# Kernel tuning notes

Hardware: AMD Instinct MI355X
Metric: run time of the kernel (lower is better)

The kernel has to match this reference:

```python
import jax, jax.numpy as jnp
import numpy as np

N = 50000        # nodes
E = 800000       # edges (before self-loops)
F_IN = 128       # num_features
HID = 32         # hidden_size per head
HEADS = 4
CLS = 40         # num_classes
NEG_SLOPE = 0.2  # PyG GATConv default leaky_relu slope


def setup_inputs() -> dict:
    key = jax.random.key(0)
    ks = jax.random.split(key, 10)
    s = lambda k, sh: (jax.random.normal(k, sh, jnp.float32) * 0.05)
    x = jax.random.normal(ks[0], (N, F_IN), jnp.float32)
    edge_index = jax.random.randint(ks[1], (2, E), 0, N, dtype=jnp.int64)
    W1 = s(ks[2], (F_IN, HEADS * HID))
    att_src1 = s(ks[3], (HEADS, HID))
    att_dst1 = s(ks[4], (HEADS, HID))
    b1 = jnp.zeros((HEADS * HID,), jnp.float32)
    W2 = s(ks[5], (HEADS * HID, CLS))
    att_src2 = s(ks[6], (1, CLS))
    att_dst2 = s(ks[7], (1, CLS))
    b2 = jnp.zeros((CLS,), jnp.float32)
    return {"x": x, "edge_index": edge_index, "W1": W1, "att_src1": att_src1,
            "att_dst1": att_dst1, "b1": b1, "W2": W2, "att_src2": att_src2,
            "att_dst2": att_dst2, "b2": b2}


def _add_self_loops(edge_index, num_nodes):
    ar = jnp.arange(num_nodes, dtype=edge_index.dtype)
    loops = jnp.stack([ar, ar])
    return jnp.concatenate([edge_index, loops], axis=1)


def _gat_conv(x, edge_index, W, a_src, a_dst, bias, heads, concat):
    """PyG GATConv (eval mode, additive attention, self-loops already added)."""
    n = x.shape[0]
    src, dst = edge_index[0], edge_index[1]
    h = (x @ W).reshape(n, heads, -1)                 # [N, H, C]
    a_s = jnp.einsum('nhc,hc->nh', h, a_src)          # [N, H]
    a_d = jnp.einsum('nhc,hc->nh', h, a_dst)          # [N, H]
    e = jax.nn.leaky_relu(a_s[src] + a_d[dst], NEG_SLOPE)   # [E', H]
    m = jax.ops.segment_max(e, dst, num_segments=n)   # segment softmax over dst
    ex = jnp.exp(e - m[dst])
    den = jax.ops.segment_sum(ex, dst, num_segments=n)
    alpha = ex / den[dst]                             # [E', H]
    out = jax.ops.segment_sum(h[src] * alpha[:, :, None], dst, num_segments=n)
    out = out.reshape(n, -1) if concat else out.mean(axis=1)
    return out + bias


def reference(x, edge_index, W1, att_src1, att_dst1, b1, W2, att_src2, att_dst2, b2):
    ei = _add_self_loops(edge_index, x.shape[0])
    # dropout p=0 in eval -> identity
    h = jax.nn.relu(_gat_conv(x, ei, W1, att_src1, att_dst1, b1, HEADS, True))
    out = _gat_conv(h, ei, W2, att_src2, att_dst2, b2, 1, True)  # heads=1
    return out
```

## Files before the change

### kernel.cpp

```cpp
#include <hip/hip_runtime.h>
#include <cstdint>

#define NODES 50000
#define FIN   128
#define C1    128
#define HEADS 4
#define HID   32
#define CLS   40
#define SLOPE 0.2f

#define NBUCK ((NODES + 255) >> 8)
#define EPB 2048
#define BCAP 8192

__device__ __forceinline__ float lrelu(float v) { return v > 0.f ? v : SLOPE * v; }

__device__ __forceinline__ unsigned short f2bf(float f) {
    union { float f; unsigned u; } v; v.f = f;
    unsigned u = v.u;
    return (unsigned short)((u + 0x7FFFu + ((u >> 16) & 1u)) >> 16);
}
__device__ __forceinline__ float bf2f(unsigned short b) {
    union { unsigned u; float f; } v; v.u = ((unsigned)b) << 16;
    return v.f;
}
__device__ __forceinline__ float bflo(unsigned u) {
    union { unsigned x; float f; } v; v.x = u << 16; return v.f;
}
__device__ __forceinline__ float bfhi(unsigned u) {
    union { unsigned x; float f; } v; v.x = u & 0xffff0000u; return v.f;
}

typedef __attribute__((ext_vector_type(8))) short bf16x8;
typedef __attribute__((ext_vector_type(4))) float f32x4;
typedef __attribute__((ext_vector_type(4), aligned(4))) int int4a;
typedef __attribute__((ext_vector_type(2), aligned(4))) int int2a;

__global__ __launch_bounds__(256) void k_prep(const float* __restrict__ W1,
                                              const float* __restrict__ W2,
                                              unsigned short* __restrict__ w1t,
                                              unsigned short* __restrict__ w2t,
                                              int* __restrict__ bwp) {
    __shared__ unsigned short Tb[128][136];
    const int t = threadIdx.x;
#pragma unroll
    for (int i = 0; i < 64; i++) {
        int p = i * 256 + t;
        int k = p >> 7, n = p & 127;
        Tb[n][k] = f2bf(W1[(size_t)k * C1 + n]);
    }
    __syncthreads();
#pragma unroll
    for (int i = 0; i < 8; i++) {
        int p = i * 256 + t;
        int n = p >> 4, k8 = (p & 15) * 8;
        *(uint4*)(w1t + n * 128 + k8) = *(uint4*)(&Tb[n][k8]);
    }
    for (int p = t; p < CLS * 128; p += 256) {
        int n = p >> 7, k = p & 127;
        w2t[n * 128 + k] = f2bf(W2[(size_t)k * CLS + n]);
    }
    if (t < NBUCK) bwp[t] = t * BCAP;
}

__global__ __launch_bounds__(256) void k_gemm1(const float* __restrict__ X,
                                               const unsigned short* __restrict__ w1t,
                                               const float* __restrict__ AS,
                                               const float* __restrict__ AD,
                                               unsigned short* __restrict__ h1b,
                                               float* __restrict__ as1,
                                               float* __restrict__ ad1) {
    __shared__ unsigned short Asm[64][136];
    __shared__ unsigned short Wt[128][136];
    const int t = threadIdx.x;
    const int row0 = blockIdx.x * 64;

#pragma unroll
    for (int i = 0; i < 8; i++) {
        int p = i * 256 + t;
        int n = p >> 4, k8 = (p & 15) * 8;
        *(uint4*)(&Wt[n][k8]) = *(const uint4*)(w1t + n * 128 + k8);
    }
    {
        int r = t >> 2, c0 = (t & 3) * 32;
        int gr = row0 + r;
        unsigned short tb[32];
        if (gr < NODES) {
#pragma unroll
            for (int i = 0; i < 8; i++) {
                float4 v = *(const float4*)(X + (size_t)gr * FIN + c0 + i * 4);
                tb[i * 4 + 0] = f2bf(v.x); tb[i * 4 + 1] = f2bf(v.y);
                tb[i * 4 + 2] = f2bf(v.z); tb[i * 4 + 3] = f2bf(v.w);
            }
        } else {
#pragma unroll
            for (int i = 0; i < 32; i++) tb[i] = 0;
        }
#pragma unroll
        for (int i = 0; i < 4; i++) {
            uint4 pk;
            pk.x = (unsigned)tb[i*8+0] | ((unsigned)tb[i*8+1] << 16);
            pk.y = (unsigned)tb[i*8+2] | ((unsigned)tb[i*8+3] << 16);
            pk.z = (unsigned)tb[i*8+4] | ((unsigned)tb[i*8+5] << 16);
            pk.w = (unsigned)tb[i*8+6] | ((unsigned)tb[i*8+7] << 16);
            *(uint4*)(&Asm[r][c0 + i * 8]) = pk;
        }
    }
    __syncthreads();

    const int w = t >> 6, l = t & 63;
    const int lm = l & 15, quad = l >> 4;
    f32x4 acc[8];
#pragma unroll
    for (int ct = 0; ct < 8; ct++) acc[ct] = (f32x4){0.f, 0.f, 0.f, 0.f};
#pragma unroll
    for (int kt = 0; kt < 4; kt++) {
        bf16x8 a = *(const bf16x8*)(&Asm[w * 16 + lm][kt * 32 + quad * 8]);
#pragma unroll
        for (int ct = 0; ct < 8; ct++) {
            bf16x8 b = *(const bf16x8*)(&Wt[ct * 16 + lm][kt * 32 + quad * 8]);
            acc[ct] = __builtin_amdgcn_mfma_f32_16x16x32_bf16(a, b, acc[ct], 0, 0, 0);
        }
    }
    __syncthreads();
#pragma unroll
    for (int ct = 0; ct < 8; ct++)
#pragma unroll
        for (int r = 0; r < 4; r++)
            Asm[w * 16 + quad * 4 + r][ct * 16 + lm] = f2bf(acc[ct][r]);
    __syncthreads();
    {
        int r = t >> 2, c0 = (t & 3) * 32;
        int gr = row0 + r;
        if (gr < NODES) {
#pragma unroll
            for (int i = 0; i < 4; i++)
                *(uint4*)(h1b + (size_t)gr * C1 + c0 + i * 8) =
                    *(uint4*)(&Asm[r][c0 + i * 8]);
        }
    }
    {
        int r = t >> 2, h = t & 3;
        int gr = row0 + r;
        if (gr < NODES) {
            float s = 0.f, d = 0.f;
#pragma unroll
            for (int j = 0; j < 32; j++) {
                float v = bf2f(Asm[r][h * 32 + j]);
                s = fmaf(v, AS[h * HID + j], s);
                d = fmaf(v, AD[h * HID + j], d);
            }
            as1[gr * HEADS + h] = s;
            ad1[gr * HEADS + h] = d;
        }
    }
}

__global__ __launch_bounds__(256) void k_bucketA(const int* __restrict__ src,
                                                 const int* __restrict__ dst, int E,
                                                 int* __restrict__ bwp,
                                                 int* __restrict__ tmp) {
    __shared__ int cnt[NBUCK];
    __shared__ int bbs[NBUCK];
    const int t = threadIdx.x;
    for (int i = t; i < NBUCK; i += 256) cnt[i] = 0;
    __syncthreads();
    const int e0 = blockIdx.x * EPB;
    int v[8], rb[8];
#pragma unroll
    for (int k = 0; k < 8; k++) {
        int e = e0 + k * 256 + t;
        rb[k] = -1;
        if (e < E) {
            int d = dst[e], s = src[e];
            int b = d >> 8;
            int r = atomicAdd(&cnt[b], 1);
            v[k] = (s << 8) | (d & 255);
            rb[k] = (r << 8) | b;
        }
    }
    __syncthreads();
    for (int i = t; i < NBUCK; i += 256) {
        int c = cnt[i];
        bbs[i] = c ? atomicAdd(&bwp[i], c) : 0;
    }
    __syncthreads();
#pragma unroll
    for (int k = 0; k < 8; k++) {
        if (rb[k] >= 0) {
            int b = rb[k] & 255;
            int r = rb[k] >> 8;
            tmp[bbs[b] + r] = v[k];
        }
    }
}

__global__ __launch_bounds__(256) void k_bucketB(const int* __restrict__ bwp,
                                                 const int* __restrict__ tmp,
                                                 int* __restrict__ col,
                                                 int* __restrict__ rowptr,
                                                 int* __restrict__ degarr) {
    __shared__ int degs[256];
    __shared__ int wp[256];
    __shared__ int wsum[4];
    const int b = blockIdx.x, t = threadIdx.x;
    const int n0 = b << 8;
    const int beg = b * BCAP;
    const int end = bwp[b];
    degs[t] = 0;
    __syncthreads();
    for (int e = beg + t; e < end; e += 256)
        atomicAdd(&degs[tmp[e] & 255], 1);
    __syncthreads();
    const int d = degs[t];
    int incl = d;
    const int lane = t & 63, w = t >> 6;
#pragma unroll
    for (int s = 1; s < 64; s <<= 1) {
        int u = __shfl_up(incl, s);
        if (lane >= s) incl += u;
    }
    if (lane == 63) wsum[w] = incl;
    __syncthreads();
    if (t == 0) {
        int r = 0;
#pragma unroll
        for (int i = 0; i < 4; i++) { int x = wsum[i]; wsum[i] = r; r += x; }
    }
    __syncthreads();
    const int excl = incl - d + wsum[w] + beg;
    const int nidx = n0 + t;
    if (nidx < NODES) { rowptr[nidx] = excl; degarr[nidx] = d; }
    wp[t] = excl;
    __syncthreads();
    for (int e = beg + t; e < end; e += 256) {
        int v = tmp[e];
        int p = atomicAdd(&wp[v & 255], 1);
        col[p] = v >> 8;
    }
}

__global__ __launch_bounds__(256) void k_agg1(const unsigned short* __restrict__ h1b,
                                              const float* __restrict__ as1,
                                              const float* __restrict__ ad1,
                                              const int* __restrict__ rowptr,
                                              const int* __restrict__ degarr,
                                              const int* __restrict__ col,
                                              const float* __restrict__ b1,
                                              unsigned short* __restrict__ out1) {
    int wid = (blockIdx.x * 256 + threadIdx.x) >> 6;
    if (wid >= NODES) return;
    const int lane = threadIdx.x & 63;
    const int q  = lane >> 4;
    const int ll = lane & 15;
    const int fh = ll >> 2;
    const int n = wid;
    const float adn = ad1[n * HEADS + fh];
    const int rs = rowptr[n];
    const int re = rs + degarr[n];

    float den = 0.f;
    float ac[8];
#pragma unroll
    for (int k = 0; k < 8; k++) ac[k] = 0.f;

    int base = rs;
    for (; base + 16 <= re; base += 16) {
        int4a cc = *(const int4a*)(col + base + q * 4);
        float w0 = __expf(lrelu(as1[cc.x * HEADS + fh] + adn));
        float w1 = __expf(lrelu(as1[cc.y * HEADS + fh] + adn));
        float w2 = __expf(lrelu(as1[cc.z * HEADS + fh] + adn));
        float w3 = __expf(lrelu(as1[cc.w * HEADS + fh] + adn));
        den += (w0 + w1) + (w2 + w3);
        uint4 p0 = *(const uint4*)((const char*)h1b + (((unsigned)cc.x << 8) + (unsigned)(ll << 4)));
        uint4 p1 = *(const uint4*)((const char*)h1b + (((unsigned)cc.y << 8) + (unsigned)(ll << 4)));
        uint4 p2 = *(const uint4*)((const char*)h1b + (((unsigned)cc.z << 8) + (unsigned)(ll << 4)));
        uint4 p3 = *(const uint4*)((const char*)h1b + (((unsigned)cc.w << 8) + (unsigned)(ll << 4)));
        ac[0] = fmaf(w0, bflo(p0.x), ac[0]); ac[1] = fmaf(w0, bfhi(p0.x), ac[1]);
        ac[2] = fmaf(w0, bflo(p0.y), ac[2]); ac[3] = fmaf(w0, bfhi(p0.y), ac[3]);
        ac[4] = fmaf(w0, bflo(p0.z), ac[4]); ac[5] = fmaf(w0, bfhi(p0.z), ac[5]);
        ac[6] = fmaf(w0, bflo(p0.w), ac[6]); ac[7] = fmaf(w0, bfhi(p0.w), ac[7]);
        ac[0] = fmaf(w1, bflo(p1.x), ac[0]); ac[1] = fmaf(w1, bfhi(p1.x), ac[1]);
        ac[2] = fmaf(w1, bflo(p1.y), ac[2]); ac[3] = fmaf(w1, bfhi(p1.y), ac[3]);
        ac[4] = fmaf(w1, bflo(p1.z), ac[4]); ac[5] = fmaf(w1, bfhi(p1.z), ac[5]);
        ac[6] = fmaf(w1, bflo(p1.w), ac[6]); ac[7] = fmaf(w1, bfhi(p1.w), ac[7]);
        ac[0] = fmaf(w2, bflo(p2.x), ac[0]); ac[1] = fmaf(w2, bfhi(p2.x), ac[1]);
        ac[2] = fmaf(w2, bflo(p2.y), ac[2]); ac[3] = fmaf(w2, bfhi(p2.y), ac[3]);
        ac[4] = fmaf(w2, bflo(p2.z), ac[4]); ac[5] = fmaf(w2, bfhi(p2.z), ac[5]);
        ac[6] = fmaf(w2, bflo(p2.w), ac[6]); ac[7] = fmaf(w2, bfhi(p2.w), ac[7]);
        ac[0] = fmaf(w3, bflo(p3.x), ac[0]); ac[1] = fmaf(w3, bfhi(p3.x), ac[1]);
        ac[2] = fmaf(w3, bflo(p3.y), ac[2]); ac[3] = fmaf(w3, bfhi(p3.y), ac[3]);
        ac[4] = fmaf(w3, bflo(p3.z), ac[4]); ac[5] = fmaf(w3, bfhi(p3.z), ac[5]);
        ac[6] = fmaf(w3, bflo(p3.w), ac[6]); ac[7] = fmaf(w3, bfhi(p3.w), ac[7]);
    }
    for (; base < re; base += 4) {
        int i = base + q;
        int c = (i < re) ? col[i] : n;
        float w = __expf(lrelu(as1[c * HEADS + fh] + adn));
        if (i >= re) w = 0.f;
        den += w;
        unsigned off = ((unsigned)c << 8) + (unsigned)(ll << 4);
        uint4 pk = *(const uint4*)((const char*)h1b + off);
        ac[0] = fmaf(w, bflo(pk.x), ac[0]); ac[1] = fmaf(w, bfhi(pk.x), ac[1]);
        ac[2] = fmaf(w, bflo(pk.y), ac[2]); ac[3] = fmaf(w, bfhi(pk.y), ac[3]);
        ac[4] = fmaf(w, bflo(pk.z), ac[4]); ac[5] = fmaf(w, bfhi(pk.z), ac[5]);
        ac[6] = fmaf(w, bflo(pk.w), ac[6]); ac[7] = fmaf(w, bfhi(pk.w), ac[7]);
    }
    den += __shfl_xor(den, 16);
    den += __shfl_xor(den, 32);
#pragma unroll
    for (int k = 0; k < 8; k++) {
        ac[k] += __shfl_xor(ac[k], 16);
        ac[k] += __shfl_xor(ac[k], 32);
    }
    const float wself = __expf(lrelu(as1[n * HEADS + fh] + adn));
    den += wself;
    if (q == 0) {
        unsigned offs = ((unsigned)n << 8) + (unsigned)(ll << 4);
        uint4 sp = *(const uint4*)((const char*)h1b + offs);
        float sv[8] = {bflo(sp.x), bfhi(sp.x), bflo(sp.y), bfhi(sp.y),
                       bflo(sp.z), bfhi(sp.z), bflo(sp.w), bfhi(sp.w)};
        float4 bv0 = *(const float4*)(b1 + ll * 8);
        float4 bv1 = *(const float4*)(b1 + ll * 8 + 4);
        float bb[8] = {bv0.x, bv0.y, bv0.z, bv0.w, bv1.x, bv1.y, bv1.z, bv1.w};
        unsigned short ob[8];
#pragma unroll
        for (int k = 0; k < 8; k++)
            ob[k] = f2bf(fmaxf((ac[k] + wself * sv[k]) / den + bb[k], 0.f));
        uint4 pk;
        pk.x = (unsigned)ob[0] | ((unsigned)ob[1] << 16);
        pk.y = (unsigned)ob[2] | ((unsigned)ob[3] << 16);
        pk.z = (unsigned)ob[4] | ((unsigned)ob[5] << 16);
        pk.w = (unsigned)ob[6] | ((unsigned)ob[7] << 16);
        *(uint4*)(out1 + (size_t)n * C1 + ll * 8) = pk;
    }
}

__global__ __launch_bounds__(256) void k_gemm2(const unsigned short* __restrict__ out1b,
                                               const unsigned short* __restrict__ w2t,
                                               const float* __restrict__ AS,
                                               const float* __restrict__ AD,
                                               unsigned short* __restrict__ h2b,
                                               float* __restrict__ as2,
                                               float* __restrict__ ad2) {
    __shared__ unsigned short Asm[64][136];
    __shared__ unsigned short Wt2[48][136];
    __shared__ float Cc[64][52];
    const int t = threadIdx.x;
    const int row0 = blockIdx.x * 64;

    for (int p = t; p < 8 * 136; p += 256) Wt2[40 + p / 136][p % 136] = 0;
    for (int p = t; p < 640; p += 256) {
        int n = p >> 4, k8 = (p & 15) * 8;
        *(uint4*)(&Wt2[n][k8]) = *(const uint4*)(w2t + n * 128 + k8);
    }
    {
        int r = t >> 2, c0 = (t & 3) * 32;
        int gr = row0 + r;
        if (gr < NODES) {
#pragma unroll
            for (int i = 0; i < 4; i++)
                *(uint4*)(&Asm[r][c0 + i * 8]) =
                    *(const uint4*)(out1b + (size_t)gr * C1 + c0 + i * 8);
        } else {
            uint4 z = make_uint4(0, 0, 0, 0);
#pragma unroll
            for (int i = 0; i < 4; i++) *(uint4*)(&Asm[r][c0 + i * 8]) = z;
        }
    }
    __syncthreads();

    const int w = t >> 6, l = t & 63;
    const int lm = l & 15, quad = l >> 4;
    f32x4 acc[3];
#pragma unroll
    for (int ct = 0; ct < 3; ct++) acc[ct] = (f32x4){0.f, 0.f, 0.f, 0.f};
#pragma unroll
    for (int kt = 0; kt < 4; kt++) {
        bf16x8 a = *(const bf16x8*)(&Asm[w * 16 + lm][kt * 32 + quad * 8]);
#pragma unroll
        for (int ct = 0; ct < 3; ct++) {
            bf16x8 b = *(const bf16x8*)(&Wt2[ct * 16 + lm][kt * 32 + quad * 8]);
            acc[ct] = __builtin_amdgcn_mfma_f32_16x16x32_bf16(a, b, acc[ct], 0, 0, 0);
        }
    }
    __syncthreads();
#pragma unroll
    for (int ct = 0; ct < 3; ct++)
#pragma unroll
        for (int r = 0; r < 4; r++)
            Cc[w * 16 + quad * 4 + r][ct * 16 + lm] = acc[ct][r];
    __syncthreads();
    {
        int r = t >> 2, c0 = (t & 3) * 10;
        int gr = row0 + r;
        if (gr < NODES) {
#pragma unroll
            for (int i = 0; i < 5; i++) {
                int c = c0 + i * 2;
                unsigned pk = (unsigned)f2bf(Cc[r][c]) |
                              ((unsigned)f2bf(Cc[r][c + 1]) << 16);
                *(unsigned*)(h2b + (size_t)gr * 64 + c) = pk;
            }
            float s = 0.f, d = 0.f;
#pragma unroll
            for (int j = 0; j < 10; j++) {
                float v = Cc[r][c0 + j];
                s = fmaf(v, AS[c0 + j], s);
                d = fmaf(v, AD[c0 + j], d);
            }
            s += __shfl_xor(s, 1); s += __shfl_xor(s, 2);
            d += __shfl_xor(d, 1); d += __shfl_xor(d, 2);
            if ((t & 3) == 0) { as2[gr] = s; ad2[gr] = d; }
        }
    }
}

__global__ __launch_bounds__(256) void k_agg2(const unsigned short* __restrict__ h2b,
                                              const float* __restrict__ as2,
                                              const float* __restrict__ ad2,
                                              const int* __restrict__ rowptr,
                                              const int* __restrict__ degarr,
                                              const int* __restrict__ col,
                                              const float* __restrict__ b2,
                                              float* __restrict__ out) {
    int wid = (blockIdx.x * 256 + threadIdx.x) >> 6;
    if (wid >= NODES) return;
    const int lane = threadIdx.x & 63;
    const int q8 = lane >> 3, l8 = lane & 7;
    const int n = wid;
    const float adn = ad2[n];
    const int rs = rowptr[n];
    const int re = rs + degarr[n];

    float den = 0.f;
    float ac[8];
#pragma unroll
    for (int k = 0; k < 8; k++) ac[k] = 0.f;

    int base = rs;
    for (; base + 16 <= re; base += 16) {
        int2a cc = *(const int2a*)(col + base + q8 * 2);
        float w0 = __expf(lrelu(as2[cc.x] + adn));
        float w1 = __expf(lrelu(as2[cc.y] + adn));
        den += w0 + w1;
        if (l8 < 5) {
            unsigned o0 = ((unsigned)cc.x << 7) + (unsigned)(l8 << 4);
            unsigned o1 = ((unsigned)cc.y << 7) + (unsigned)(l8 << 4);
            uint4 p0 = *(const uint4*)((const char*)h2b + o0);
            uint4 p1 = *(const uint4*)((const char*)h2b + o1);
            ac[0] = fmaf(w0, bflo(p0.x), ac[0]); ac[1] = fmaf(w0, bfhi(p0.x), ac[1]);
            ac[2] = fmaf(w0, bflo(p0.y), ac[2]); ac[3] = fmaf(w0, bfhi(p0.y), ac[3]);
            ac[4] = fmaf(w0, bflo(p0.z), ac[4]); ac[5] = fmaf(w0, bfhi(p0.z), ac[5]);
            ac[6] = fmaf(w0, bflo(p0.w), ac[6]); ac[7] = fmaf(w0, bfhi(p0.w), ac[7]);
            ac[0] = fmaf(w1, bflo(p1.x), ac[0]); ac[1] = fmaf(w1, bfhi(p1.x), ac[1]);
            ac[2] = fmaf(w1, bflo(p1.y), ac[2]); ac[3] = fmaf(w1, bfhi(p1.y), ac[3]);
            ac[4] = fmaf(w1, bflo(p1.z), ac[4]); ac[5] = fmaf(w1, bfhi(p1.z), ac[5]);
            ac[6] = fmaf(w1, bflo(p1.w), ac[6]); ac[7] = fmaf(w1, bfhi(p1.w), ac[7]);
        }
    }
    for (; base < re; base += 8) {
        int i = base + q8;
        int c = (i < re) ? col[i] : n;
        float w = __expf(lrelu(as2[c] + adn));
        if (i >= re) w = 0.f;
        den += w;
        if (l8 < 5) {
            unsigned off = ((unsigned)c << 7) + (unsigned)(l8 << 4);
            uint4 pk = *(const uint4*)((const char*)h2b + off);
            ac[0] = fmaf(w, bflo(pk.x), ac[0]); ac[1] = fmaf(w, bfhi(pk.x), ac[1]);
            ac[2] = fmaf(w, bflo(pk.y), ac[2]); ac[3] = fmaf(w, bfhi(pk.y), ac[3]);
            ac[4] = fmaf(w, bflo(pk.z), ac[4]); ac[5] = fmaf(w, bfhi(pk.z), ac[5]);
            ac[6] = fmaf(w, bflo(pk.w), ac[6]); ac[7] = fmaf(w, bfhi(pk.w), ac[7]);
        }
    }
    den += __shfl_xor(den, 8);
    den += __shfl_xor(den, 16);
    den += __shfl_xor(den, 32);
#pragma unroll
    for (int k = 0; k < 8; k++) {
        ac[k] += __shfl_xor(ac[k], 8);
        ac[k] += __shfl_xor(ac[k], 16);
        ac[k] += __shfl_xor(ac[k], 32);
    }
    const float wself = __expf(lrelu(as2[n] + adn));
    den += wself;
    if (q8 == 0 && l8 < 5) {
        unsigned offs = ((unsigned)n << 7) + (unsigned)(l8 << 4);
        uint4 sp = *(const uint4*)((const char*)h2b + offs);
        float sv[8] = {bflo(sp.x), bfhi(sp.x), bflo(sp.y), bfhi(sp.y),
                       bflo(sp.z), bfhi(sp.z), bflo(sp.w), bfhi(sp.w)};
        float4 bv0 = *(const float4*)(b2 + l8 * 8);
        float4 bv1 = *(const float4*)(b2 + l8 * 8 + 4);
        float bb[8] = {bv0.x, bv0.y, bv0.z, bv0.w, bv1.x, bv1.y, bv1.z, bv1.w};
        float o[8];
#pragma unroll
        for (int k = 0; k < 8; k++)
            o[k] = (ac[k] + wself * sv[k]) / den + bb[k];
        *(float4*)(out + (size_t)n * CLS + l8 * 8) =
            make_float4(o[0], o[1], o[2], o[3]);
        *(float4*)(out + (size_t)n * CLS + l8 * 8 + 4) =
            make_float4(o[4], o[5], o[6], o[7]);
    }
}

extern "C" void kernel_launch(void* const* d_in, const int* in_sizes, int n_in,
                              void* d_out, int out_size, void* d_ws, size_t ws_size,
                              hipStream_t stream) {
    const float* x     = (const float*)d_in[0];
    const int*   ei    = (const int*)d_in[1];
    const float* W1    = (const float*)d_in[2];
    const float* aS1   = (const float*)d_in[3];
    const float* aD1   = (const float*)d_in[4];
    const float* b1    = (const float*)d_in[5];
    const float* W2    = (const float*)d_in[6];
    const float* aS2   = (const float*)d_in[7];
    const float* aD2   = (const float*)d_in[8];
    const float* b2    = (const float*)d_in[9];
    float* out = (float*)d_out;
    const int E = in_sizes[1] / 2;
    const int* src = ei;
    const int* dst = ei + E;

    char* ws = (char*)d_ws;
    size_t off = 0;
    auto alloc = [&](size_t bytes) -> char* {
        char* p = ws + off;
        off += (bytes + 255) & ~(size_t)255;
        return p;
    };
    unsigned short* h1b  = (unsigned short*)alloc((size_t)NODES * C1 * 2);
    unsigned short* out1 = (unsigned short*)alloc((size_t)NODES * C1 * 2);
    unsigned short* h2b  = (unsigned short*)alloc((size_t)NODES * 64 * 2);
    float* as1    = (float*)alloc((size_t)NODES * HEADS * 4);
    float* ad1    = (float*)alloc((size_t)NODES * HEADS * 4);
    float* as2    = (float*)alloc((size_t)NODES * 4);
    float* ad2    = (float*)alloc((size_t)NODES * 4);
    int* rowptr   = (int*)alloc((size_t)NODES * 4);
    int* degarr   = (int*)alloc((size_t)NODES * 4);
    int* col      = (int*)alloc((size_t)NBUCK * BCAP * 4);
    int* tmp      = (int*)alloc((size_t)NBUCK * BCAP * 4);
    unsigned short* w1t = (unsigned short*)alloc((size_t)FIN * C1 * 2);
    unsigned short* w2t = (unsigned short*)alloc((size_t)CLS * 128 * 2);
    int* bwp      = (int*)alloc((size_t)NBUCK * 4);

    k_prep<<<1, 256, 0, stream>>>(W1, W2, w1t, w2t, bwp);
    k_gemm1<<<(NODES + 63) / 64, 256, 0, stream>>>(x, w1t, aS1, aD1, h1b, as1, ad1);
    k_bucketA<<<(E + EPB - 1) / EPB, 256, 0, stream>>>(src, dst, E, bwp, tmp);
    k_bucketB<<<NBUCK, 256, 0, stream>>>(bwp, tmp, col, rowptr, degarr);
    k_agg1<<<(NODES * 64) / 256, 256, 0, stream>>>(h1b, as1, ad1, rowptr, degarr, col, b1, out1);
    k_gemm2<<<(NODES + 63) / 64, 256, 0, stream>>>(out1, w2t, aS2, aD2, h2b, as2, ad2);
    k_agg2<<<(NODES * 64) / 256, 256, 0, stream>>>(h2b, as2, ad2, rowptr, degarr, col, b2, out);
}
```

Before: 211.9 us.

## Fuse edge bucketing into GEMM1 launch and fold GEMM2 into layer-1 aggregation

Edge bucketing (formerly its own kernel) now runs as extra blocks of the first GEMM kernel, so the two independent stages share one launch and can overlap. The second-layer projection and its attention scores are computed inside the layer-1 aggregation kernel: each wave shuffles its node's 128-wide bf16 output into an MFMA A-fragment with only one valid row and multiplies by W2 staged in shared memory. This removes the out1 intermediate round-trip through global memory and one kernel launch. The cost is that every aggregation block now loads W2 into shared memory, and the MFMA does mostly zero-padded work since only one of its 16 rows is a real node.

```diff
diff --git a/kernel.cpp b/kernel.cpp
--- a/kernel.cpp
+++ b/kernel.cpp
@@ -36,6 +36,8 @@
 typedef __attribute__((ext_vector_type(4), aligned(4))) int int4a;
 typedef __attribute__((ext_vector_type(2), aligned(4))) int int2a;
 
+union BF8 { uint4 u; bf16x8 v; };
+
 __global__ __launch_bounds__(256) void k_prep(const float* __restrict__ W1,
                                               const float* __restrict__ W2,
                                               unsigned short* __restrict__ w1t,
@@ -63,18 +65,58 @@
     if (t < NBUCK) bwp[t] = t * BCAP;
 }
 
-__global__ __launch_bounds__(256) void k_gemm1(const float* __restrict__ X,
+__global__ __launch_bounds__(256) void k_front(const float* __restrict__ X,
                                                const unsigned short* __restrict__ w1t,
                                                const float* __restrict__ AS,
                                                const float* __restrict__ AD,
                                                unsigned short* __restrict__ h1b,
                                                float* __restrict__ as1,
-                                               float* __restrict__ ad1) {
+                                               float* __restrict__ ad1,
+                                               const int* __restrict__ src,
+                                               const int* __restrict__ dst, int E,
+                                               int* __restrict__ bwp,
+                                               int* __restrict__ tmp, int GB1) {
     __shared__ unsigned short Asm[64][136];
     __shared__ unsigned short Wt[128][136];
+    __shared__ int cnt[NBUCK];
+    __shared__ int bbs[NBUCK];
     const int t = threadIdx.x;
+
+    if (blockIdx.x >= GB1) {
+        for (int i = t; i < NBUCK; i += 256) cnt[i] = 0;
+        __syncthreads();
+        const int e0 = (blockIdx.x - GB1) * EPB;
+        int v[8], rb[8];
+#pragma unroll
+        for (int k = 0; k < 8; k++) {
+            int e = e0 + k * 256 + t;
+            rb[k] = -1;
+            if (e < E) {
+                int d = dst[e], s = src[e];
+                int b = d >> 8;
+                int r = atomicAdd(&cnt[b], 1);
+                v[k] = (s << 8) | (d & 255);
+                rb[k] = (r << 8) | b;
+            }
+        }
+        __syncthreads();
+        for (int i = t; i < NBUCK; i += 256) {
+            int c = cnt[i];
+            bbs[i] = c ? atomicAdd(&bwp[i], c) : 0;
+        }
+        __syncthreads();
+#pragma unroll
+        for (int k = 0; k < 8; k++) {
+            if (rb[k] >= 0) {
+                int b = rb[k] & 255;
+                int r = rb[k] >> 8;
+                tmp[bbs[b] + r] = v[k];
+            }
+        }
+        return;
+    }
+
     const int row0 = blockIdx.x * 64;
-
 #pragma unroll
     for (int i = 0; i < 8; i++) {
         int p = i * 256 + t;
@@ -152,45 +194,6 @@
             }
             as1[gr * HEADS + h] = s;
             ad1[gr * HEADS + h] = d;
-        }
-    }
-}
-
-__global__ __launch_bounds__(256) void k_bucketA(const int* __restrict__ src,
-                                                 const int* __restrict__ dst, int E,
-                                                 int* __restrict__ bwp,
-                                                 int* __restrict__ tmp) {
-    __shared__ int cnt[NBUCK];
-    __shared__ int bbs[NBUCK];
-    const int t = threadIdx.x;
-    for (int i = t; i < NBUCK; i += 256) cnt[i] = 0;
-    __syncthreads();
-    const int e0 = blockIdx.x * EPB;
-    int v[8], rb[8];
-#pragma unroll
-    for (int k = 0; k < 8; k++) {
-        int e = e0 + k * 256 + t;
-        rb[k] = -1;
-        if (e < E) {
-            int d = dst[e], s = src[e];
-            int b = d >> 8;
-            int r = atomicAdd(&cnt[b], 1);
-            v[k] = (s << 8) | (d & 255);
-            rb[k] = (r << 8) | b;
-        }
-    }
-    __syncthreads();
-    for (int i = t; i < NBUCK; i += 256) {
-        int c = cnt[i];
-        bbs[i] = c ? atomicAdd(&bwp[i], c) : 0;
-    }
-    __syncthreads();
-#pragma unroll
-    for (int k = 0; k < 8; k++) {
-        if (rb[k] >= 0) {
-            int b = rb[k] & 255;
-            int r = rb[k] >> 8;
-            tmp[bbs[b] + r] = v[k];
         }
     }
 }
@@ -247,10 +250,23 @@
                                               const int* __restrict__ degarr,
                                               const int* __restrict__ col,
                                               const float* __restrict__ b1,
-                                              unsigned short* __restrict__ out1) {
-    int wid = (blockIdx.x * 256 + threadIdx.x) >> 6;
-    if (wid >= NODES) return;
-    const int lane = threadIdx.x & 63;
+                                              const unsigned short* __restrict__ w2t,
+                                              const float* __restrict__ AS2,
+                                              const float* __restrict__ AD2,
+                                              unsigned short* __restrict__ h2b,
+                                              float* __restrict__ as2,
+                                              float* __restrict__ ad2) {
+    __shared__ unsigned short Wt2[48][136];
+    const int t = threadIdx.x;
+    for (int p = t; p < 640; p += 256) {
+        int nn = p >> 4, k8 = (p & 15) * 8;
+        *(uint4*)(&Wt2[nn][k8]) = *(const uint4*)(w2t + nn * 128 + k8);
+    }
+    for (int p = t; p < 8 * 136; p += 256) Wt2[40 + p / 136][p % 136] = 0;
+    __syncthreads();
+
+    int wid = (blockIdx.x * 256 + t) >> 6;
+    const int lane = t & 63;
     const int q  = lane >> 4;
     const int ll = lane & 15;
     const int fh = ll >> 2;
@@ -315,7 +331,9 @@
     }
     const float wself = __expf(lrelu(as1[n * HEADS + fh] + adn));
     den += wself;
-    if (q == 0) {
+
+    unsigned pk01, pk23, pk45, pk67;
+    {
         unsigned offs = ((unsigned)n << 8) + (unsigned)(ll << 4);
         uint4 sp = *(const uint4*)((const char*)h1b + offs);
         float sv[8] = {bflo(sp.x), bfhi(sp.x), bflo(sp.y), bfhi(sp.y),
@@ -323,97 +341,50 @@
         float4 bv0 = *(const float4*)(b1 + ll * 8);
         float4 bv1 = *(const float4*)(b1 + ll * 8 + 4);
         float bb[8] = {bv0.x, bv0.y, bv0.z, bv0.w, bv1.x, bv1.y, bv1.z, bv1.w};
-        unsigned short ob[8];
+        float o[8];
 #pragma unroll
         for (int k = 0; k < 8; k++)
-            ob[k] = f2bf(fmaxf((ac[k] + wself * sv[k]) / den + bb[k], 0.f));
-        uint4 pk;
-        pk.x = (unsigned)ob[0] | ((unsigned)ob[1] << 16);
-        pk.y = (unsigned)ob[2] | ((unsigned)ob[3] << 16);
-        pk.z = (unsigned)ob[4] | ((unsigned)ob[5] << 16);
-        pk.w = (unsigned)ob[6] | ((unsigned)ob[7] << 16);
-        *(uint4*)(out1 + (size_t)n * C1 + ll * 8) = pk;
-    }
-}
-
-__global__ __launch_bounds__(256) void k_gemm2(const unsigned short* __restrict__ out1b,
-                                               const unsigned short* __restrict__ w2t,
-                                               const float* __restrict__ AS,
-                                               const float* __restrict__ AD,
-                                               unsigned short* __restrict__ h2b,
-                                               float* __restrict__ as2,
-                                               float* __restrict__ ad2) {
-    __shared__ unsigned short Asm[64][136];
-    __shared__ unsigned short Wt2[48][136];
-    __shared__ float Cc[64][52];
-    const int t = threadIdx.x;
-    const int row0 = blockIdx.x * 64;
-
-    for (int p = t; p < 8 * 136; p += 256) Wt2[40 + p / 136][p % 136] = 0;
-    for (int p = t; p < 640; p += 256) {
-        int n = p >> 4, k8 = (p & 15) * 8;
-        *(uint4*)(&Wt2[n][k8]) = *(const uint4*)(w2t + n * 128 + k8);
-    }
-    {
-        int r = t >> 2, c0 = (t & 3) * 32;
-        int gr = row0 + r;
-        if (gr < NODES) {
-#pragma unroll
-            for (int i = 0; i < 4; i++)
-                *(uint4*)(&Asm[r][c0 + i * 8]) =
-                    *(const uint4*)(out1b + (size_t)gr * C1 + c0 + i * 8);
-        } else {
-            uint4 z = make_uint4(0, 0, 0, 0);
-#pragma unroll
-            for (int i = 0; i < 4; i++) *(uint4*)(&Asm[r][c0 + i * 8]) = z;
-        }
-    }
-    __syncthreads();
-
-    const int w = t >> 6, l = t & 63;
-    const int lm = l & 15, quad = l >> 4;
-    f32x4 acc[3];
-#pragma unroll
-    for (int ct = 0; ct < 3; ct++) acc[ct] = (f32x4){0.f, 0.f, 0.f, 0.f};
+            o[k] = fmaxf((ac[k] + wself * sv[k]) / den + bb[k], 0.f);
+        pk01 = (unsigned)f2bf(o[0]) | ((unsigned)f2bf(o[1]) << 16);
+        pk23 = (unsigned)f2bf(o[2]) | ((unsigned)f2bf(o[3]) << 16);
+        pk45 = (unsigned)f2bf(o[4]) | ((unsigned)f2bf(o[5]) << 16);
+        pk67 = (unsigned)f2bf(o[6]) | ((unsigned)f2bf(o[7]) << 16);
+    }
+    f32x4 a2[3];
+#pragma unroll
+    for (int ct = 0; ct < 3; ct++) a2[ct] = (f32x4){0.f, 0.f, 0.f, 0.f};
 #pragma unroll
     for (int kt = 0; kt < 4; kt++) {
-        bf16x8 a = *(const bf16x8*)(&Asm[w * 16 + lm][kt * 32 + quad * 8]);
+        int sl = kt * 4 + q;
+        BF8 af;
+        af.u.x = (unsigned)__shfl((int)pk01, sl);
+        af.u.y = (unsigned)__shfl((int)pk23, sl);
+        af.u.z = (unsigned)__shfl((int)pk45, sl);
+        af.u.w = (unsigned)__shfl((int)pk67, sl);
+        if (ll != 0) af.u = make_uint4(0, 0, 0, 0);
 #pragma unroll
         for (int ct = 0; ct < 3; ct++) {
-            bf16x8 b = *(const bf16x8*)(&Wt2[ct * 16 + lm][kt * 32 + quad * 8]);
-            acc[ct] = __builtin_amdgcn_mfma_f32_16x16x32_bf16(a, b, acc[ct], 0, 0, 0);
-        }
-    }
-    __syncthreads();
-#pragma unroll
-    for (int ct = 0; ct < 3; ct++)
-#pragma unroll
-        for (int r = 0; r < 4; r++)
-            Cc[w * 16 + quad * 4 + r][ct * 16 + lm] = acc[ct][r];
-    __syncthreads();
-    {
-        int r = t >> 2, c0 = (t & 3) * 10;
-        int gr = row0 + r;
-        if (gr < NODES) {
-#pragma unroll
-            for (int i = 0; i < 5; i++) {
-                int c = c0 + i * 2;
-                unsigned pk = (unsigned)f2bf(Cc[r][c]) |
-                              ((unsigned)f2bf(Cc[r][c + 1]) << 16);
-                *(unsigned*)(h2b + (size_t)gr * 64 + c) = pk;
-            }
-            float s = 0.f, d = 0.f;
-#pragma unroll
-            for (int j = 0; j < 10; j++) {
-                float v = Cc[r][c0 + j];
-                s = fmaf(v, AS[c0 + j], s);
-                d = fmaf(v, AD[c0 + j], d);
-            }
-            s += __shfl_xor(s, 1); s += __shfl_xor(s, 2);
-            d += __shfl_xor(d, 1); d += __shfl_xor(d, 2);
-            if ((t & 3) == 0) { as2[gr] = s; ad2[gr] = d; }
-        }
-    }
+            bf16x8 b = *(const bf16x8*)(&Wt2[ct * 16 + ll][kt * 32 + q * 8]);
+            a2[ct] = __builtin_amdgcn_mfma_f32_16x16x32_bf16(af.v, b, a2[ct], 0, 0, 0);
+        }
+    }
+    float s = 0.f, d = 0.f;
+#pragma unroll
+    for (int ct = 0; ct < 3; ct++) {
+        int c = ct * 16 + ll;
+        float hv = a2[ct][0];
+        if (c < CLS) {
+            if (q == 0) h2b[(size_t)n * 64 + c] = f2bf(hv);
+            s = fmaf(hv, AS2[c], s);
+            d = fmaf(hv, AD2[c], d);
+        }
+    }
+#pragma unroll
+    for (int dd = 1; dd < 64; dd <<= 1) {
+        s += __shfl_xor(s, dd);
+        d += __shfl_xor(d, dd);
+    }
+    if (lane == 0) { as2[n] = s; ad2[n] = d; }
 }
 
 __global__ __launch_bounds__(256) void k_agg2(const unsigned short* __restrict__ h2b,
@@ -530,7 +501,6 @@
         return p;
     };
     unsigned short* h1b  = (unsigned short*)alloc((size_t)NODES * C1 * 2);
-    unsigned short* out1 = (unsigned short*)alloc((size_t)NODES * C1 * 2);
     unsigned short* h2b  = (unsigned short*)alloc((size_t)NODES * 64 * 2);
     float* as1    = (float*)alloc((size_t)NODES * HEADS * 4);
     float* ad1    = (float*)alloc((size_t)NODES * HEADS * 4);
@@ -544,11 +514,16 @@
     unsigned short* w2t = (unsigned short*)alloc((size_t)CLS * 128 * 2);
     int* bwp      = (int*)alloc((size_t)NBUCK * 4);
 
+    const int GB1 = (NODES + 63) / 64;
+    const int GBA = (E + EPB - 1) / EPB;
+
     k_prep<<<1, 256, 0, stream>>>(W1, W2, w1t, w2t, bwp);
-    k_gemm1<<<(NODES + 63) / 64, 256, 0, stream>>>(x, w1t, aS1, aD1, h1b, as1, ad1);
-    k_bucketA<<<(E + EPB - 1) / EPB, 256, 0, stream>>>(src, dst, E, bwp, tmp);
+    k_front<<<GB1 + GBA, 256, 0, stream>>>(x, w1t, aS1, aD1, h1b, as1, ad1,
+                                           src, dst, E, bwp, tmp, GB1);
     k_bucketB<<<NBUCK, 256, 0, stream>>>(bwp, tmp, col, rowptr, degarr);
-    k_agg1<<<(NODES * 64) / 256, 256, 0, stream>>>(h1b, as1, ad1, rowptr, degarr, col, b1, out1);
-    k_gemm2<<<(NODES + 63) / 64, 256, 0, stream>>>(out1, w2t, aS2, aD2, h2b, as2, ad2);
-    k_agg2<<<(NODES * 64) / 256, 256, 0, stream>>>(h2b, as2, ad2, rowptr, degarr, col, b2, out);
-}
+    k_agg1<<<(NODES * 64) / 256, 256, 0, stream>>>(h1b, as1, ad1, rowptr, degarr,
+                                                   col, b1, w2t, aS2, aD2,
+                                                   h2b, as2, ad2);
+    k_agg2<<<(NODES * 64) / 256, 256, 0, stream>>>(h2b, as2, ad2, rowptr, degarr,
+                                                   col, b2, out);
+}
```

Result: slower. 219.9 us (+3.7%).
